# Performance work log

Hardware: AMD Instinct MI355X
Metric: run time of the kernel (lower is better)

Reference implementation:

```python
import jax, jax.numpy as jnp
import numpy as np

LEVELS = 3  # num_basis = 1 + 1 + 2 + 4 = 8


def _haar_basis(x):
    """Closed-form vectorized Haar basis, x: [B, F] raw inputs.

    Replaces the original nested per-feature/per-level/per-bucket mask loops:
    at each level only one bucket k = floor(u*freq) is active, with value
    +2^(level/2) on the left half of the bucket and -2^(level/2) on the right
    half (x == 1.0 falls in the right half of the last bucket, matching the
    torch edge-case handling).
    """
    u = (jnp.tanh(x) + 1.0) / 2.0  # normalize to [0, 1]
    cols = [jnp.ones_like(u)[..., None]]  # scaling function phi
    for level in range(LEVELS):
        freq = 2 ** level
        k = jnp.clip(jnp.floor(u * freq), 0, freq - 1).astype(jnp.int32)  # bucket idx
        mid = (k.astype(u.dtype) + 0.5) / freq
        amp = jnp.asarray(2.0 ** (level / 2), u.dtype)
        sign = jnp.where(u < mid, amp, -amp)  # [B, F]
        cols.append(jax.nn.one_hot(k, freq, dtype=u.dtype) * sign[..., None])
    return jnp.concatenate(cols, axis=-1)  # [B, F, num_basis]


def setup_inputs() -> dict:
    key = jax.random.key(0)
    k1, k2, k3 = jax.random.split(key, 3)
    B, F, O, NB = 32768, 1024, 64, 8
    x = jax.random.normal(k1, (B, F), dtype=jnp.float32)
    coeffs = jax.random.normal(k2, (F, O, NB), dtype=jnp.float32) * 0.05
    base_weight = jax.random.normal(k3, (F, O), dtype=jnp.float32) * 0.05
    return {"x": x, "coeffs": coeffs, "base_weight": base_weight}


def reference(x, coeffs, base_weight):
    basis = _haar_basis(x)                         # [B, F, NB]
    wave_out = jnp.einsum('bin,ion->bo', basis, coeffs)  # [B, O]
    out = wave_out + x @ base_weight               # residual path
    kl = jnp.zeros((1,), dtype=x.dtype)            # non-variational: kl = 0
    return (out, kl)
```

## Files before the change

### kernel.cpp

```cpp
#include <hip/hip_runtime.h>
#include <math.h>


typedef __attribute__((ext_vector_type(8))) short short8;
typedef __attribute__((ext_vector_type(4))) float f32x4;
typedef __attribute__((ext_vector_type(16))) float f32x16;

__device__ __forceinline__ unsigned int f2bf(float f) {
  unsigned int u = __float_as_uint(f);
  u += 0x7FFFu + ((u >> 16) & 1u);
  return u >> 16;
}

__device__ __forceinline__ void gen_basis(int j, unsigned int* d) {
  d[0] = (j < 4) ? 0x3F803F80u : 0xBF803F80u;
  unsigned int sq1 = (j & 2) ? 0xBFB5u : 0x3FB5u;
  d[1] = (j & 4) ? (sq1 << 16) : sq1;
  unsigned long long sd2 = (j & 1) ? 0xC000ull : 0x4000ull;
  unsigned long long d23 = sd2 << ((j & 6) << 3);
  d[2] = (unsigned int)d23;
  d[3] = (unsigned int)(d23 >> 32);
}

__global__ __launch_bounds__(256) void build_w(const float* __restrict__ coeffs,
                                               const float* __restrict__ bw,
                                               uint4* __restrict__ Wsw) {
  const int l = threadIdx.x & 63;
  const int t = threadIdx.x >> 6;
  const int g = blockIdx.x;
  const int c = g / 9, j = g - c * 9;
  const int u = t >> 1, nq = t & 1;
  const int R = c * 4 + 2 * u + (l >> 5);
  const int o = nq * 32 + (l & 31);
  unsigned int dwv[4];
#pragma unroll
  for (int jj = 0; jj < 8; ++jj) {
    int f, n;
    if (j < 8) { f = 8 * R + j;  n = jj; }
    else       { f = 8 * R + jj; n = 8;  }
    float v = (n < 8) ? coeffs[(f * 64 + o) * 8 + n] : bw[f * 64 + o];
    unsigned int hh = f2bf(v);
    if (jj & 1) dwv[jj >> 1] |= hh << 16; else dwv[jj >> 1] = hh;
  }
  uint4 qq; qq.x = dwv[0]; qq.y = dwv[1]; qq.z = dwv[2]; qq.w = dwv[3];
  Wsw[(g * 4 + t) * 64 + l] = qq;
}

#define MFMA32(A, B, C) __builtin_amdgcn_mfma_f32_32x32x16_bf16( \
    __builtin_bit_cast(short8, (A)), __builtin_bit_cast(short8, (B)), (C), 0, 0, 0)

__global__ __launch_bounds__(512, 4) void wavelet_gemm(const float* __restrict__ x,
                                                       const uint4* __restrict__ Bsw,
                                                       float* __restrict__ out,
                                                       int out_size) {
  __shared__ float P[4 * 4096];
  const int tid = threadIdx.x;
  const int l = tid & 63;
  const int w = tid >> 6;
  const int ks = w >> 1;
  const int mh = w & 1;
  const int hi = l >> 5;
  const int l31 = l & 31;
  const long rowbase = (long)blockIdx.x * 64;
  const float* xr = x + (rowbase + mh * 32 + l31) * 1024;
  const int sA = 2 * ks;
  const int xduty = (ks < 2);
  const int xrun = 2 * ks + hi;

  f32x16 acc0 = {};
  f32x16 acc1 = {};

#pragma unroll 1
  for (int c = 0; c < 32; ++c) {
    const int cb = 32 * c;
    const uint4* wp = Bsw + ((size_t)(c * 9 + sA) * 4) * 64 + l;
    uint4 BA0 = wp[0],   BA1 = wp[64],  BA2 = wp[128], BA3 = wp[192];
    uint4 BB0 = wp[256], BB1 = wp[320], BB2 = wp[384], BB3 = wp[448];
    float2 f20 = *(const float2*)(xr + cb + 8 * hi + sA);
    float2 f21 = *(const float2*)(xr + cb + 8 * (2 + hi) + sA);

    float xv[4] = {f20.x, f20.y, f21.x, f21.y};
    float t8v[4];
    unsigned int bad = 0;
#pragma unroll
    for (int ff = 0; ff < 4; ++ff) {
      float e = __expf(2.0f * xv[ff]);
      float r = __builtin_amdgcn_rcpf(e + 1.0f);
      float t8 = __builtin_fmaf(-8.0f, r, 8.0f);
      float rn = rintf(t8);
      if (fabsf(t8 - rn) < 3e-5f) bad |= 1u << ff;
      t8v[ff] = t8;
    }
    if (__builtin_expect(bad != 0, 0)) {
#pragma unroll
      for (int ff = 0; ff < 4; ++ff)
        if (bad & (1u << ff)) {
          float tf = (float)tanh((double)xv[ff]);
          t8v[ff] = ((tf + 1.0f) * 0.5f) * 8.0f;
        }
    }
    uint4 A[4];
#pragma unroll
    for (int ff = 0; ff < 4; ++ff) {
      int j = (int)t8v[ff]; j = j > 7 ? 7 : j;
      unsigned int d[4];
      gen_basis(j, d);
      A[ff].x = d[0]; A[ff].y = d[1]; A[ff].z = d[2]; A[ff].w = d[3];
    }
    acc0 = MFMA32(A[0], BA0, acc0);
    acc1 = MFMA32(A[0], BA1, acc1);
    acc0 = MFMA32(A[2], BA2, acc0);
    acc1 = MFMA32(A[2], BA3, acc1);
    acc0 = MFMA32(A[1], BB0, acc0);
    acc1 = MFMA32(A[1], BB1, acc1);
    acc0 = MFMA32(A[3], BB2, acc0);
    acc1 = MFMA32(A[3], BB3, acc1);
    if (xduty) {
      const uint4* wx = Bsw + ((size_t)(c * 9 + 8) * 4) * 64 + l;
      uint4 BXa = wx[(2 * ks) * 64];
      uint4 BXb = wx[(2 * ks + 1) * 64];
      float4 xo0 = *(const float4*)(xr + cb + 8 * xrun);
      float4 xo1 = *(const float4*)(xr + cb + 8 * xrun + 4);
      uint4 xa;
      xa.x = f2bf(xo0.x) | (f2bf(xo0.y) << 16);
      xa.y = f2bf(xo0.z) | (f2bf(xo0.w) << 16);
      xa.z = f2bf(xo1.x) | (f2bf(xo1.y) << 16);
      xa.w = f2bf(xo1.z) | (f2bf(xo1.w) << 16);
      acc0 = MFMA32(xa, BXa, acc0);
      acc1 = MFMA32(xa, BXb, acc1);
    }
  }

  float* Pk = P + ks * 4096;
  const int rbase = 32 * mh + 4 * hi;
#pragma unroll
  for (int rg = 0; rg < 16; ++rg) {
    const int grow = (rg & 3) + 8 * (rg >> 2) + rbase;
    Pk[grow * 64 + l31]      = acc0[rg];
    Pk[grow * 64 + 32 + l31] = acc1[rg];
  }
  __syncthreads();

  float* og = out + (size_t)rowbase * 64;
  const int d = tid * 4;
  f32x4 v0 = *(const f32x4*)(P + d) + *(const f32x4*)(P + 4096 + d)
           + *(const f32x4*)(P + 8192 + d) + *(const f32x4*)(P + 12288 + d);
  f32x4 v1 = *(const f32x4*)(P + 2048 + d) + *(const f32x4*)(P + 6144 + d)
           + *(const f32x4*)(P + 10240 + d) + *(const f32x4*)(P + 14336 + d);
  *(f32x4*)(og + d) = v0;
  *(f32x4*)(og + 2048 + d) = v1;
  if (blockIdx.x == 0 && tid == 0) out[out_size - 1] = 0.0f;
}

extern "C" void kernel_launch(void* const* d_in, const int* in_sizes, int n_in,
                              void* d_out, int out_size, void* d_ws, size_t ws_size,
                              hipStream_t stream) {
  const float* x      = (const float*)d_in[0];
  const float* coeffs = (const float*)d_in[1];
  const float* bw     = (const float*)d_in[2];
  uint4* Wsw = (uint4*)d_ws;
  float* out = (float*)d_out;

  build_w<<<288, 256, 0, stream>>>(coeffs, bw, Wsw);
  wavelet_gemm<<<512, 512, 0, stream>>>(x, (const uint4*)Wsw, out, out_size);
}
```

Baseline: 271.9 us.

## Stage x tiles through double-buffered LDS with coalesced prefetch

Each block now loads its 64x32 slice of x per chunk cooperatively with coalesced float4 loads into a padded, double-buffered LDS tile. The next chunk is prefetched into registers during compute, and every wave reads its x values from LDS instead of issuing strided per-row global loads. This is meant to cut uncoalesced global traffic and duplicate x reads across waves. The cost is a block-wide barrier every iteration, extra LDS traffic, and scalar stores into the padded tile.

New measurement: 277.5 us. +2.1%, slower.

```diff
diff --git a/kernel.cpp b/kernel.cpp
--- a/kernel.cpp
+++ b/kernel.cpp
@@ -21,6 +21,8 @@
   d[2] = (unsigned int)d23;
   d[3] = (unsigned int)(d23 >> 32);
 }
+
+#define BARRIER() __asm__ volatile("s_waitcnt lgkmcnt(0)\n\ts_barrier" ::: "memory")
 
 __global__ __launch_bounds__(256) void build_w(const float* __restrict__ coeffs,
                                                const float* __restrict__ bw,
@@ -53,7 +55,9 @@
                                                        const uint4* __restrict__ Bsw,
                                                        float* __restrict__ out,
                                                        int out_size) {
-  __shared__ float P[4 * 4096];
+  __shared__ float LDSu[4 * 4096];
+  float* const XT0 = LDSu;
+  float* const XT1 = LDSu + 64 * 33;
   const int tid = threadIdx.x;
   const int l = tid & 63;
   const int w = tid >> 6;
@@ -62,24 +66,40 @@
   const int hi = l >> 5;
   const int l31 = l & 31;
   const long rowbase = (long)blockIdx.x * 64;
-  const float* xr = x + (rowbase + mh * 32 + l31) * 1024;
   const int sA = 2 * ks;
   const int xduty = (ks < 2);
   const int xrun = 2 * ks + hi;
 
+  const int srow = tid >> 3;
+  const int scol = (tid & 7) * 4;
+  const float* sp = x + (rowbase + srow) * 1024 + scol;
+  float* const sd0 = XT0 + srow * 33 + scol;
+  float* const sd1 = XT1 + srow * 33 + scol;
+
+  const float* const xrow_lds0 = XT0 + (32 * mh + l31) * 33;
+  const float* const xrow_lds1 = XT1 + (32 * mh + l31) * 33;
+
   f32x16 acc0 = {};
   f32x16 acc1 = {};
 
+  {
+    float4 g0 = *(const float4*)(sp);
+    sd0[0] = g0.x; sd0[1] = g0.y; sd0[2] = g0.z; sd0[3] = g0.w;
+  }
+  BARRIER();
+
 #pragma unroll 1
   for (int c = 0; c < 32; ++c) {
-    const int cb = 32 * c;
     const uint4* wp = Bsw + ((size_t)(c * 9 + sA) * 4) * 64 + l;
     uint4 BA0 = wp[0],   BA1 = wp[64],  BA2 = wp[128], BA3 = wp[192];
     uint4 BB0 = wp[256], BB1 = wp[320], BB2 = wp[384], BB3 = wp[448];
-    float2 f20 = *(const float2*)(xr + cb + 8 * hi + sA);
-    float2 f21 = *(const float2*)(xr + cb + 8 * (2 + hi) + sA);
+    float4 gn;
+    if (c + 1 < 32) gn = *(const float4*)(sp + 32 * (c + 1));
+    const float* Xc = (c & 1) ? xrow_lds1 : xrow_lds0;
+    float xv[4];
+    xv[0] = Xc[8 * hi + sA];       xv[1] = Xc[8 * hi + sA + 1];
+    xv[2] = Xc[8 * (2 + hi) + sA]; xv[3] = Xc[8 * (2 + hi) + sA + 1];
 
-    float xv[4] = {f20.x, f20.y, f21.x, f21.y};
     float t8v[4];
     unsigned int bad = 0;
 #pragma unroll
@@ -119,18 +139,25 @@
       const uint4* wx = Bsw + ((size_t)(c * 9 + 8) * 4) * 64 + l;
       uint4 BXa = wx[(2 * ks) * 64];
       uint4 BXb = wx[(2 * ks + 1) * 64];
-      float4 xo0 = *(const float4*)(xr + cb + 8 * xrun);
-      float4 xo1 = *(const float4*)(xr + cb + 8 * xrun + 4);
+      float xo[8];
+#pragma unroll
+      for (int i = 0; i < 8; ++i) xo[i] = Xc[8 * xrun + i];
       uint4 xa;
-      xa.x = f2bf(xo0.x) | (f2bf(xo0.y) << 16);
-      xa.y = f2bf(xo0.z) | (f2bf(xo0.w) << 16);
-      xa.z = f2bf(xo1.x) | (f2bf(xo1.y) << 16);
-      xa.w = f2bf(xo1.z) | (f2bf(xo1.w) << 16);
+      xa.x = f2bf(xo[0]) | (f2bf(xo[1]) << 16);
+      xa.y = f2bf(xo[2]) | (f2bf(xo[3]) << 16);
+      xa.z = f2bf(xo[4]) | (f2bf(xo[5]) << 16);
+      xa.w = f2bf(xo[6]) | (f2bf(xo[7]) << 16);
       acc0 = MFMA32(xa, BXa, acc0);
       acc1 = MFMA32(xa, BXb, acc1);
     }
+    if (c + 1 < 32) {
+      float* sd = ((c + 1) & 1) ? sd1 : sd0;
+      sd[0] = gn.x; sd[1] = gn.y; sd[2] = gn.z; sd[3] = gn.w;
+    }
+    BARRIER();
   }
 
+  float* P = LDSu;
   float* Pk = P + ks * 4096;
   const int rbase = 32 * mh + 4 * hi;
 #pragma unroll
```

## Stage Haar basis tiles in double-buffered LDS and rebalance K-split across waves

Applied to the files above, without the earlier changes.

Each block now covers 32 rows with 4 waves. Every thread builds the basis and bf16 x fragments once per chunk into a double-buffered LDS tile, so the basis is no longer recomputed per MFMA consumer. Waves split the 9 K-slices (wave 0 takes 3, the others 2), and the next chunk is built while MFMAs run on the current one, with setprio raised around the MFMA section. This removes the redundant transcendental work and the uneven x-path duty of the old layout. In exchange it adds LDS traffic and a barrier per chunk, and the grid grows to 1024 blocks.

Measured after the change: 269.4 us. No clear change (-0.9%).

```diff
diff --git a/kernel.cpp b/kernel.cpp
--- a/kernel.cpp
+++ b/kernel.cpp
@@ -20,6 +20,45 @@
   unsigned long long d23 = sd2 << ((j & 6) << 3);
   d[2] = (unsigned int)d23;
   d[3] = (unsigned int)(d23 >> 32);
+}
+
+#define BARRIER() __asm__ volatile("s_waitcnt lgkmcnt(0)\n\ts_barrier" ::: "memory")
+
+__device__ __forceinline__ void build_half(const float4& xq, uint4* __restrict__ buf,
+                                           int run, int row, int h) {
+  float xv[4] = {xq.x, xq.y, xq.z, xq.w};
+  float t8v[4];
+  unsigned int bad = 0;
+#pragma unroll
+  for (int ff = 0; ff < 4; ++ff) {
+    float e = __expf(2.0f * xv[ff]);
+    float r = __builtin_amdgcn_rcpf(e + 1.0f);
+    float t8 = __builtin_fmaf(-8.0f, r, 8.0f);
+    float rn = rintf(t8);
+    if (fabsf(t8 - rn) < 3e-5f) bad |= 1u << ff;
+    t8v[ff] = t8;
+  }
+  if (__builtin_expect(bad != 0, 0)) {
+#pragma unroll
+    for (int ff = 0; ff < 4; ++ff)
+      if (bad & (1u << ff)) {
+        float tf = (float)tanh((double)xv[ff]);
+        t8v[ff] = ((tf + 1.0f) * 0.5f) * 8.0f;
+      }
+  }
+  uint4* dq = buf + run * 32 + row;
+#pragma unroll
+  for (int k = 0; k < 4; ++k) {
+    int j = (int)t8v[k]; j = j > 7 ? 7 : j;
+    unsigned int d[4];
+    gen_basis(j, d);
+    uint4 qv; qv.x = d[0]; qv.y = d[1]; qv.z = d[2]; qv.w = d[3];
+    dq[(4 * h + k) * 128] = qv;
+  }
+  uint2 hv;
+  hv.x = f2bf(xv[0]) | (f2bf(xv[1]) << 16);
+  hv.y = f2bf(xv[2]) | (f2bf(xv[3]) << 16);
+  ((uint2*)(buf + 8 * 128 + run * 32 + row))[h] = hv;
 }
 
 __global__ __launch_bounds__(256) void build_w(const float* __restrict__ coeffs,
@@ -49,106 +88,91 @@
 #define MFMA32(A, B, C) __builtin_amdgcn_mfma_f32_32x32x16_bf16( \
     __builtin_bit_cast(short8, (A)), __builtin_bit_cast(short8, (B)), (C), 0, 0, 0)
 
-__global__ __launch_bounds__(512, 4) void wavelet_gemm(const float* __restrict__ x,
+template <int NS>
+__device__ __forceinline__ void run_main(const float* __restrict__ xrow,
+                                         const uint4* __restrict__ Bsw,
+                                         uint4* __restrict__ Albuf,
+                                         f32x16& acc0, f32x16& acc1,
+                                         int ks, int l, int run, int row_b, int h) {
+  const int hi = l >> 5;
+  const int l31 = l & 31;
+  float4 xa = *(const float4*)(xrow);
+  build_half(xa, Albuf, run, row_b, h);
+  xa = *(const float4*)(xrow + 32);
+  BARRIER();
+
+  for (int c = 0; c < 32; ++c) {
+    uint4* cur = Albuf + (c & 1) * 1152;
+    uint4* nxt = Albuf + ((c + 1) & 1) * 1152;
+    uint4 Bv[NS][4];
+#pragma unroll
+    for (int i = 0; i < NS; ++i) {
+      const uint4* wp = Bsw + ((size_t)((c * 9 + ks + 4 * i) * 4)) * 64 + l;
+      Bv[i][0] = wp[0]; Bv[i][1] = wp[64]; Bv[i][2] = wp[128]; Bv[i][3] = wp[192];
+    }
+    if (c + 1 < 32) {
+      build_half(xa, nxt, run, row_b, h);
+      if (c + 2 < 32) xa = *(const float4*)(xrow + (c + 2) * 32);
+    }
+    __builtin_amdgcn_s_setprio(1);
+#pragma unroll
+    for (int i = 0; i < NS; ++i) {
+      const int s = ks + 4 * i;
+      const uint4* rb = cur + s * 128;
+      uint4 a0 = rb[hi * 32 + l31];
+      uint4 a1 = rb[(2 + hi) * 32 + l31];
+      acc0 = MFMA32(a0, Bv[i][0], acc0);
+      acc1 = MFMA32(a0, Bv[i][1], acc1);
+      acc0 = MFMA32(a1, Bv[i][2], acc0);
+      acc1 = MFMA32(a1, Bv[i][3], acc1);
+    }
+    __builtin_amdgcn_s_setprio(0);
+    BARRIER();
+  }
+}
+
+__global__ __launch_bounds__(256, 4) void wavelet_gemm(const float* __restrict__ x,
                                                        const uint4* __restrict__ Bsw,
                                                        float* __restrict__ out,
                                                        int out_size) {
-  __shared__ float P[4 * 4096];
+  __shared__ uint4 Albuf[2 * 1152];
   const int tid = threadIdx.x;
   const int l = tid & 63;
   const int w = tid >> 6;
-  const int ks = w >> 1;
-  const int mh = w & 1;
-  const int hi = l >> 5;
-  const int l31 = l & 31;
-  const long rowbase = (long)blockIdx.x * 64;
-  const float* xr = x + (rowbase + mh * 32 + l31) * 1024;
-  const int sA = 2 * ks;
-  const int xduty = (ks < 2);
-  const int xrun = 2 * ks + hi;
+  const int ks = w;
+  const int run = w;
+  const int row_b = l >> 1;
+  const int h = l & 1;
+  const long rowbase = (long)blockIdx.x * 32;
 
   f32x16 acc0 = {};
   f32x16 acc1 = {};
 
-#pragma unroll 1
-  for (int c = 0; c < 32; ++c) {
-    const int cb = 32 * c;
-    const uint4* wp = Bsw + ((size_t)(c * 9 + sA) * 4) * 64 + l;
-    uint4 BA0 = wp[0],   BA1 = wp[64],  BA2 = wp[128], BA3 = wp[192];
-    uint4 BB0 = wp[256], BB1 = wp[320], BB2 = wp[384], BB3 = wp[448];
-    float2 f20 = *(const float2*)(xr + cb + 8 * hi + sA);
-    float2 f21 = *(const float2*)(xr + cb + 8 * (2 + hi) + sA);
+  const float* xrow = x + (rowbase + row_b) * 1024 + run * 8 + h * 4;
 
-    float xv[4] = {f20.x, f20.y, f21.x, f21.y};
-    float t8v[4];
-    unsigned int bad = 0;
-#pragma unroll
-    for (int ff = 0; ff < 4; ++ff) {
-      float e = __expf(2.0f * xv[ff]);
-      float r = __builtin_amdgcn_rcpf(e + 1.0f);
-      float t8 = __builtin_fmaf(-8.0f, r, 8.0f);
-      float rn = rintf(t8);
-      if (fabsf(t8 - rn) < 3e-5f) bad |= 1u << ff;
-      t8v[ff] = t8;
-    }
-    if (__builtin_expect(bad != 0, 0)) {
-#pragma unroll
-      for (int ff = 0; ff < 4; ++ff)
-        if (bad & (1u << ff)) {
-          float tf = (float)tanh((double)xv[ff]);
-          t8v[ff] = ((tf + 1.0f) * 0.5f) * 8.0f;
-        }
-    }
-    uint4 A[4];
-#pragma unroll
-    for (int ff = 0; ff < 4; ++ff) {
-      int j = (int)t8v[ff]; j = j > 7 ? 7 : j;
-      unsigned int d[4];
-      gen_basis(j, d);
-      A[ff].x = d[0]; A[ff].y = d[1]; A[ff].z = d[2]; A[ff].w = d[3];
-    }
-    acc0 = MFMA32(A[0], BA0, acc0);
-    acc1 = MFMA32(A[0], BA1, acc1);
-    acc0 = MFMA32(A[2], BA2, acc0);
-    acc1 = MFMA32(A[2], BA3, acc1);
-    acc0 = MFMA32(A[1], BB0, acc0);
-    acc1 = MFMA32(A[1], BB1, acc1);
-    acc0 = MFMA32(A[3], BB2, acc0);
-    acc1 = MFMA32(A[3], BB3, acc1);
-    if (xduty) {
-      const uint4* wx = Bsw + ((size_t)(c * 9 + 8) * 4) * 64 + l;
-      uint4 BXa = wx[(2 * ks) * 64];
-      uint4 BXb = wx[(2 * ks + 1) * 64];
-      float4 xo0 = *(const float4*)(xr + cb + 8 * xrun);
-      float4 xo1 = *(const float4*)(xr + cb + 8 * xrun + 4);
-      uint4 xa;
-      xa.x = f2bf(xo0.x) | (f2bf(xo0.y) << 16);
-      xa.y = f2bf(xo0.z) | (f2bf(xo0.w) << 16);
-      xa.z = f2bf(xo1.x) | (f2bf(xo1.y) << 16);
-      xa.w = f2bf(xo1.z) | (f2bf(xo1.w) << 16);
-      acc0 = MFMA32(xa, BXa, acc0);
-      acc1 = MFMA32(xa, BXb, acc1);
-    }
-  }
+  if (w == 0) run_main<3>(xrow, Bsw, Albuf, acc0, acc1, 0,  l, run, row_b, h);
+  else        run_main<2>(xrow, Bsw, Albuf, acc0, acc1, ks, l, run, row_b, h);
 
-  float* Pk = P + ks * 4096;
-  const int rbase = 32 * mh + 4 * hi;
+  float* P = (float*)Albuf;
+  float* Pk = P + ks * 2048;
+  const int l31 = l & 31;
+  const int rbase = 4 * (l >> 5);
 #pragma unroll
   for (int rg = 0; rg < 16; ++rg) {
     const int grow = (rg & 3) + 8 * (rg >> 2) + rbase;
     Pk[grow * 64 + l31]      = acc0[rg];
     Pk[grow * 64 + 32 + l31] = acc1[rg];
   }
-  __syncthreads();
+  BARRIER();
 
   float* og = out + (size_t)rowbase * 64;
-  const int d = tid * 4;
-  f32x4 v0 = *(const f32x4*)(P + d) + *(const f32x4*)(P + 4096 + d)
-           + *(const f32x4*)(P + 8192 + d) + *(const f32x4*)(P + 12288 + d);
-  f32x4 v1 = *(const f32x4*)(P + 2048 + d) + *(const f32x4*)(P + 6144 + d)
-           + *(const f32x4*)(P + 10240 + d) + *(const f32x4*)(P + 14336 + d);
+  const int d = tid * 8;
+  f32x4 v0 = *(const f32x4*)(P + d)     + *(const f32x4*)(P + 2048 + d)
+           + *(const f32x4*)(P + 4096 + d) + *(const f32x4*)(P + 6144 + d);
+  f32x4 v1 = *(const f32x4*)(P + d + 4) + *(const f32x4*)(P + 2048 + d + 4)
+           + *(const f32x4*)(P + 4096 + d + 4) + *(const f32x4*)(P + 6144 + d + 4);
   *(f32x4*)(og + d) = v0;
-  *(f32x4*)(og + 2048 + d) = v1;
+  *(f32x4*)(og + d + 4) = v1;
   if (blockIdx.x == 0 && tid == 0) out[out_size - 1] = 0.0f;
 }
 
@@ -162,5 +186,5 @@
   float* out = (float*)d_out;
 
   build_w<<<288, 256, 0, stream>>>(coeffs, bw, Wsw);
-  wavelet_gemm<<<512, 512, 0, stream>>>(x, (const uint4*)Wsw, out, out_size);
+  wavelet_gemm<<<1024, 256, 0, stream>>>(x, (const uint4*)Wsw, out, out_size);
 }
```
